# Optimization experiments

Measured on AMD Instinct MI355X. Metric: run time of the kernel, lower is better.

## Reference

```python
import jax, jax.numpy as jnp
import numpy as np

B, N, D = 64, 1024, 512
H, LD = 8, 64            # num_heads, linear_hidden_dim (H*LD == D)
HIDDEN = 4 * D           # ffn_multiply = 4.0
NB = 128                 # number of timestamp buckets
EPS = 1e-6
TS_SCALE = NB / 14.0     # log1p(1e6) ~ 13.8 -> buckets span [0, NB]


def rms_norm(x, eps=EPS):
    return x * jax.lax.rsqrt(jnp.mean(x * x, axis=-1, keepdims=True) + eps)


def setup_inputs() -> dict:
    key = jax.random.key(0)
    ks = jax.random.split(key, 8)
    lengths = np.linspace(256, N, B).astype(np.int64)
    x_offsets = jnp.asarray(np.concatenate([[0], np.cumsum(lengths)]), dtype=jnp.int64)
    T = int(lengths.sum())
    x = jax.random.normal(ks[0], (T, D), dtype=jnp.float32)
    all_timestamps = jnp.sort(jax.random.randint(ks[1], (B, N), 0, 10**6, dtype=jnp.int64), axis=1)
    invalid_attn_mask = jnp.tril(jnp.ones((N, N), jnp.float32))  # causal
    uv = jax.random.normal(ks[2], (D, 3 * H * LD), dtype=jnp.float32) * 0.02
    pos_w = jax.random.normal(ks[3], (2 * N - 1,), dtype=jnp.float32) * 0.02
    ts_w = jax.random.normal(ks[4], (NB + 1,), dtype=jnp.float32) * 0.02
    w_ams = jax.random.normal(ks[5], (2 * H * LD, D), dtype=jnp.float32) * 0.02
    w1 = jax.random.normal(ks[6], (D, HIDDEN), dtype=jnp.float32) * 0.02
    w2 = jax.random.normal(ks[7], (HIDDEN, D), dtype=jnp.float32) * 0.02
    return {"x": x, "x_offsets": x_offsets, "all_timestamps": all_timestamps,
            "invalid_attn_mask": invalid_attn_mask, "uv": uv, "pos_w": pos_w,
            "ts_w": ts_w, "w_ams": w_ams, "w1": w1, "w2": w2}


def reference(x, x_offsets, all_timestamps, invalid_attn_mask, uv, pos_w, ts_w, w_ams, w1, w2):
    T = x.shape[0]
    # RMSNorm (no learned scale, matches F.rms_norm with no weight) + fused proj + SiLU
    proj = jax.nn.silu(rms_norm(x) @ uv)                       # [T, 3*H*LD]
    u, v = proj[:, :2 * H * LD], proj[:, 2 * H * LD:]          # [T,2HD'], [T,HD']
    # jagged -> padded dense
    tok = jnp.arange(T)
    seg = jnp.searchsorted(x_offsets, tok, side="right") - 1   # batch id per token
    pos = tok - x_offsets[seg]                                  # position within sequence
    padded_v = jnp.zeros((B, N, H * LD), v.dtype).at[seg, pos].set(v).reshape(B, N, H, LD)
    # positional relative bias (batch-independent)
    rel = jnp.arange(N)[:, None] - jnp.arange(N)[None, :]
    pos_attn = pos_w[rel + N - 1] * invalid_attn_mask           # [N,N]
    # temporal relative bias: log-bucketized |t_i - t_j|
    dt = jnp.abs(all_timestamps[:, :, None] - all_timestamps[:, None, :]).astype(jnp.float32)
    bucket = jnp.clip(jnp.floor(jnp.log1p(dt) * TS_SCALE), 0, NB).astype(jnp.int32)
    ts_attn = ts_w[bucket] * invalid_attn_mask[None]            # [B,N,N]
    # two-stream bias 'attention' (no softmax)
    out_pos = jnp.einsum("nm,bmhd->bnhd", pos_attn, padded_v)
    out_ts = jnp.einsum("bnm,bmhd->bnhd", ts_attn, padded_v)
    combined = jnp.concatenate([out_pos, out_ts], axis=-1).reshape(B, N, 2 * H * LD)
    attn_out = combined[seg, pos]                               # dense -> jagged, [T, 2*H*LD]
    # gated norm + multistage FFN with residuals
    ams = u * rms_norm(attn_out)
    h = x + ams @ w_ams
    out = h + jax.nn.silu(rms_norm(h) @ w1) @ w2
    return out
```

## Files before the change

kernel.cpp:

```cpp
#include <hip/hip_runtime.h>
#include <cmath>


using u16 = unsigned short;
using u8  = unsigned char;

typedef __bf16 bf16x8 __attribute__((ext_vector_type(8)));
typedef __bf16 bf16x2 __attribute__((ext_vector_type(2)));
typedef float  f32x4  __attribute__((ext_vector_type(4)));
typedef float  f32x2  __attribute__((ext_vector_type(2)));

#define TS_SCALE_F (float)(128.0 / 14.0)

__device__ __forceinline__ u16 f2b(float f) {
  unsigned u = __float_as_uint(f);
  unsigned r = 0x7FFFu + ((u >> 16) & 1u);
  return (u16)((u + r) >> 16);
}
__device__ __forceinline__ u16 f2b_n(float f) {
  union { __bf16 b; u16 u; } c; c.b = (__bf16)f; return c.u;
}
__device__ __forceinline__ unsigned cvt_pk2(float a, float b) {
  f32x2 v; v[0] = a; v[1] = b;
  bf16x2 r = __builtin_convertvector(v, bf16x2);
  union { bf16x2 b; unsigned u; } c; c.b = r; return c.u;
}
__device__ __forceinline__ float b2f(u16 v) {
  return __uint_as_float(((unsigned)v) << 16);
}
__device__ __forceinline__ bf16x8 as_frag(uint4 r) {
  union { uint4 u; bf16x8 v; } c; c.u = r; return c.v;
}

__device__ __forceinline__ void gload_lds16(const u16* g, u16* l) {
  __builtin_amdgcn_global_load_lds(
      (const __attribute__((address_space(1))) unsigned int*)g,
      (__attribute__((address_space(3))) unsigned int*)l, 16, 0, 0);
}

__device__ __forceinline__ size_t ts_base_u8(int b, int nt) {
  return (size_t)b * 589824 + (size_t)(nt * (nt + 1) / 2) * 16384;
}

__global__ __launch_bounds__(256) void wprep(
    const float* __restrict__ W, u16* __restrict__ Wp, int K, int N)
{
  const int p = blockIdx.x, s = blockIdx.y;
  const int t = threadIdx.x;
  size_t base = ((size_t)p * (K >> 5) + s) * 4096;
  const int e0 = t * 16;
  u16 o[16];
#pragma unroll
  for (int i = 0; i < 16; ++i) {
    int e = e0 + i;
    int kb = e >> 10, r = e & 1023, c = r >> 3, ke = r & 7;
    o[i] = f2b(W[(size_t)(s * 32 + kb * 8 + ke) * N + p * 128 + c]);
  }
  *(uint4*)(Wp + base + e0)     = *(uint4*)o;
  *(uint4*)(Wp + base + e0 + 8) = *(uint4*)(o + 8);
}

#define EPI_SILU_BF16  0
#define EPI_ADD_F32    1
#define EPI_ADDS       3
#define EPI_SILUSC_IMG 4
#define AM_BF16   0
#define AM_IMG    3
#define AM_BF16M  5

template <int EPI, int AMODE>
__global__ __launch_bounds__(256, 2) void gemm_bf16(
    const u16* __restrict__ A,
    const float* __restrict__ inv, const u16* __restrict__ U, int ustride,
    const u16* __restrict__ Wp, void* __restrict__ C,
    const float* __restrict__ ADD,
    int M, int N, int K, int ncb)
{
  __shared__ u16 lA[128 * 40];
  __shared__ u16 lB[4096];

  const int nblk = gridDim.x;
  const int q = nblk >> 3, r = nblk & 7;
  const int xcd = blockIdx.x & 7, li = blockIdx.x >> 3;
  const int work = xcd * q + (xcd < r ? xcd : r) + li;
  const int c0b = work % ncb;
  const int t0  = (work / ncb) * 128;
  const int c0  = c0b * 128;

  const int tid  = threadIdx.x;
  const int wave = tid >> 6, lane = tid & 63;
  const int wr   = (wave >> 1) * 64, wc = (wave & 1) * 64;
  const int l15  = lane & 15, l4 = lane >> 4;

  f32x4 z = {0.f, 0.f, 0.f, 0.f};
  f32x4 acc[4][4];
#pragma unroll
  for (int m = 0; m < 4; ++m)
#pragma unroll
    for (int j = 0; j < 4; ++j) acc[m][j] = z;

  const int ar = tid >> 1, ak = (tid & 1) * 16;
  const int row = t0 + ar;
  const bool arow_ok = row < M;
  const u16* ab = (AMODE == AM_BF16 || AMODE == AM_BF16M)
                      ? A + (size_t)row * K + ak : nullptr;
  const u16* um = (AMODE == AM_BF16M)
                      ? U + (size_t)row * ustride + ak : nullptr;

  const int ksteps = K >> 5;
  const u16* wsrc = Wp + (size_t)c0b * ksteps * 4096 + wave * 1024 + lane * 8;
  u16* ldsb = &lB[wave * 1024];
  const u16* asrc = (AMODE == AM_IMG)
      ? A + (size_t)(t0 >> 7) * ksteps * 4096 + wave * 1024 + lane * 8
      : nullptr;
  u16* ldsa = &lA[wave * 1024];

  for (int s = 0; s < ksteps; ++s) {
    gload_lds16(wsrc,       ldsb);
    gload_lds16(wsrc + 512, ldsb + 512);
    wsrc += 4096;
    if constexpr (AMODE == AM_IMG) {
      gload_lds16(asrc,       ldsa);
      gload_lds16(asrc + 512, ldsa + 512);
      asrc += 4096;
    } else {
      const int k0 = s * 32;
      uint4 pr[4];
      const uint4 z4 = make_uint4(0, 0, 0, 0);
      if (!arow_ok) { pr[0] = z4; pr[1] = z4; pr[2] = z4; pr[3] = z4; }
      else if constexpr (AMODE == AM_BF16) {
        pr[0] = *(const uint4*)(ab + k0);
        pr[1] = *(const uint4*)(ab + k0 + 8);
      } else {
        pr[0] = *(const uint4*)(ab + k0);
        pr[1] = *(const uint4*)(ab + k0 + 8);
        pr[2] = *(const uint4*)(um + k0);
        pr[3] = *(const uint4*)(um + k0 + 8);
      }
      u16 tmp[16];
      unsigned* t32 = (unsigned*)tmp;
      if constexpr (AMODE == AM_BF16) {
        *(uint4*)tmp       = pr[0];
        *(uint4*)(tmp + 8) = pr[1];
      } else {
        const u16* a = (const u16*)pr;
        const u16* u = (const u16*)(pr + 2);
#pragma unroll
        for (int i = 0; i < 8; ++i)
          t32[i] = cvt_pk2(b2f(a[2 * i]) * b2f(u[2 * i]),
                           b2f(a[2 * i + 1]) * b2f(u[2 * i + 1]));
      }
      *(uint4*)&lA[ar * 40 + ak]     = *(uint4*)tmp;
      *(uint4*)&lA[ar * 40 + ak + 8] = *(uint4*)(tmp + 8);
    }
    __syncthreads();

    bf16x8 afr[4], bfv[4];
#pragma unroll
    for (int m = 0; m < 4; ++m) {
      if constexpr (AMODE == AM_IMG)
        afr[m] = as_frag(*(const uint4*)&lA[(l4 << 10) + (wr + m * 16 + l15) * 8]);
      else
        afr[m] = as_frag(*(const uint4*)&lA[(wr + m * 16 + l15) * 40 + l4 * 8]);
    }
#pragma unroll
    for (int j = 0; j < 4; ++j)
      bfv[j] = as_frag(*(const uint4*)&lB[(l4 << 10) + (wc + j * 16 + l15) * 8]);
#pragma unroll
    for (int m = 0; m < 4; ++m)
#pragma unroll
      for (int j = 0; j < 4; ++j)
        acc[m][j] = __builtin_amdgcn_mfma_f32_16x16x32_bf16(afr[m], bfv[j], acc[m][j], 0, 0, 0);
    __syncthreads();
  }

#pragma unroll
  for (int m = 0; m < 4; ++m) {
#pragma unroll
    for (int rr = 0; rr < 4; ++rr) {
      int orow = t0 + wr + m * 16 + l4 * 4 + rr;
      if (orow >= M) continue;
      float einv = 0.f;
      if (EPI == EPI_ADDS || EPI == EPI_SILUSC_IMG) einv = inv[orow];
#pragma unroll
      for (int j = 0; j < 4; ++j) {
        int col = c0 + wc + j * 16 + l15;
        float y = acc[m][j][rr];
        if constexpr (EPI == EPI_SILU_BF16) {
          float s = y / (1.f + __expf(-y));
          ((u16*)C)[(size_t)orow * N + col] = f2b_n(s);
        } else if constexpr (EPI == EPI_ADD_F32) {
          size_t idx = (size_t)orow * N + col;
          ((float*)C)[idx] = y + ADD[idx];
        } else if constexpr (EPI == EPI_ADDS) {
          size_t idx = (size_t)orow * N + col;
          ((float*)C)[idx] = y * einv + ADD[idx];
        } else {
          float y2 = y * einv;
          float s = y2 / (1.f + __expf(-y2));
          size_t ioff = ((size_t)(t0 >> 7) * (N >> 5) + (col >> 5)) * 4096
                      + (size_t)((col >> 3) & 3) * 1024
                      + (size_t)(orow & 127) * 8 + (col & 7);
          ((u16*)C)[ioff] = f2b_n(s);
        }
      }
    }
  }
}

__global__ __launch_bounds__(128) void pos_scores(
    const float* __restrict__ pos_w, u16* __restrict__ pos_s)
{
  const int n = blockIdx.x;
  const int m0 = threadIdx.x * 8;
  u16 o[8];
#pragma unroll
  for (int i = 0; i < 8; ++i) {
    int m = m0 + i;
    float v = (m <= n) ? pos_w[n - m + 1023] : 0.f;
    o[i] = f2b(v);
  }
  *(uint4*)(pos_s + (size_t)n * 1024 + m0) = *(uint4*)o;
}

__global__ __launch_bounds__(256) void ts_buckets(
    const int* __restrict__ tstamp, u8* __restrict__ ts_s)
{
  const int nt = 7 - (blockIdx.x >> 6);
  const int b  = blockIdx.x & 63;
  const int W  = 128 * (nt + 1);
  const int n0 = nt * 128;
  const int tid = threadIdx.x;

  __shared__ int tsm[1024];
  for (int i = tid; i < W; i += 256) tsm[i] = tstamp[b * 1024 + i];
  __syncthreads();

  const int r = tid >> 1, h = tid & 1;
  const int n_abs = n0 + r;
  const int t_n = tstamp[b * 1024 + n_abs];
  const int half = W >> 1;
  const int c0 = h * half;
  u8* row = ts_s + ts_base_u8(b, nt) + (size_t)r * W + c0;

  for (int c = 0; c < half; c += 16) {
    u8 o[16];
#pragma unroll
    for (int i = 0; i < 16; ++i) {
      int m = c0 + c + i;
      int d = t_n - tsm[m];
      if (d < 0) d = -d;
      int bkt = (int)(log1pf((float)d) * TS_SCALE_F);
      bkt = bkt > 128 ? 128 : bkt;
      o[i] = (m <= n_abs) ? (u8)bkt : (u8)129;
    }
    *(uint4*)(row + c) = *(uint4*)o;
  }
}

__global__ __launch_bounds__(256, 1) void attn_gemm(
    const u16* __restrict__ proj,
    const int* __restrict__ xoff,
    const u16* __restrict__ pos_s,
    const u8*  __restrict__ tsU8,
    const float* __restrict__ ts_w,
    u16* __restrict__ attn_out,
    int Ttot)
{
  const int flat = blockIdx.x;
  const int nt = 7 - (flat >> 8);
  const int rem = flat & 255;
  const int b  = rem >> 2;
  const int ct = rem & 3;

  const int off = xoff[b];
  int len = xoff[b + 1] - off;
  if (len < 0) len = 0;
  if (len > 1024) len = 1024;
  if (off < 0 || off + len > Ttot) return;
  const int n0 = nt * 128;
  if (n0 >= len) return;
  const int c0 = ct * 128;
  const int W = 128 * (nt + 1);

  __shared__ u16 lP[128 * 40];
  __shared__ u16 lT[128 * 40];
  __shared__ u16 sV[4096];
  __shared__ float s_tsw[130];

  const int tid = threadIdx.x;
  if (tid < 130) s_tsw[tid] = (tid < 129) ? ts_w[tid] : 0.f;
  __syncthreads();

  const int wave = tid >> 6, lane = tid & 63;
  const int wr = (wave >> 1) * 64, wc = (wave & 1) * 64;
  const int l15 = lane & 15, l4 = lane >> 4;

  f32x4 z = {0.f, 0.f, 0.f, 0.f};
  f32x4 accP[4][4], accT[4][4];
#pragma unroll
  for (int m = 0; m < 4; ++m)
#pragma unroll
    for (int j = 0; j < 4; ++j) { accP[m][j] = z; accT[m][j] = z; }

  const int ar = tid >> 1, ak = (tid & 1) * 16;
  const u16* pRow = pos_s + (size_t)(n0 + ar) * 1024 + ak;
  const u8*  tRow = tsU8 + ts_base_u8(b, nt) + (size_t)ar * W + ak;
  const int vk = tid >> 3, vc = (tid & 7) * 16;

  const int mEnd = (n0 + 128 < len) ? (n0 + 128) : len;

  for (int m0 = 0; m0 < mEnd; m0 += 32) {
    {
      int mm = m0 + vk;
      uint4 v0 = make_uint4(0, 0, 0, 0), v1 = v0;
      if (mm < len) {
        const u16* src = proj + (size_t)(off + mm) * 1536 + 1024 + c0 + vc;
        v0 = *(const uint4*)src;
        v1 = *(const uint4*)(src + 8);
      }
      u16 tmp[16];
      *(uint4*)tmp       = v0;
      *(uint4*)(tmp + 8) = v1;
      const int kb = vk >> 3, ke = vk & 7;
#pragma unroll
      for (int i = 0; i < 16; ++i) {
        int col = vc + i;
        int o2 = (kb * 2048 + col * 16 + ke * 2) ^ (((col >> 3) & 7) << 4);
        *(u16*)((char*)sV + o2) = tmp[i];
      }
    }
    {
      uint4 p0 = *(const uint4*)(pRow + m0);
      uint4 p1 = *(const uint4*)(pRow + m0 + 8);
      uint4 tb = *(const uint4*)(tRow + m0);
      const u8* bp = (const u8*)&tb;
      unsigned tt32[8];
#pragma unroll
      for (int i = 0; i < 8; ++i)
        tt32[i] = cvt_pk2(s_tsw[bp[2 * i]], s_tsw[bp[2 * i + 1]]);
      int wb = ar * 40 + ak;
      *(uint4*)&lP[wb]     = p0;
      *(uint4*)&lP[wb + 8] = p1;
      *(uint4*)&lT[wb]     = *(uint4*)tt32;
      *(uint4*)&lT[wb + 8] = *(uint4*)(tt32 + 4);
    }
    __syncthreads();

    bf16x8 ap[4], at[4], bv[4];
#pragma unroll
    for (int m = 0; m < 4; ++m) {
      ap[m] = as_frag(*(const uint4*)&lP[(wr + m * 16 + l15) * 40 + l4 * 8]);
      at[m] = as_frag(*(const uint4*)&lT[(wr + m * 16 + l15) * 40 + l4 * 8]);
    }
#pragma unroll
    for (int j = 0; j < 4; ++j) {
      int col = wc + j * 16 + l15;
      int o2 = (l4 * 2048 + col * 16) ^ (((col >> 3) & 7) << 4);
      bv[j] = as_frag(*(const uint4*)((char*)sV + o2));
    }
#pragma unroll
    for (int m = 0; m < 4; ++m)
#pragma unroll
      for (int j = 0; j < 4; ++j) {
        accP[m][j] = __builtin_amdgcn_mfma_f32_16x16x32_bf16(ap[m], bv[j], accP[m][j], 0, 0, 0);
        accT[m][j] = __builtin_amdgcn_mfma_f32_16x16x32_bf16(at[m], bv[j], accT[m][j], 0, 0, 0);
      }
    __syncthreads();
  }

#pragma unroll
  for (int m = 0; m < 4; ++m)
#pragma unroll
    for (int r = 0; r < 4; ++r) {
      int n = n0 + wr + m * 16 + l4 * 4 + r;
      if (n >= len) continue;
      size_t t = (size_t)(off + n);
#pragma unroll
      for (int j = 0; j < 4; ++j) {
        int hd = c0 + wc + j * 16 + l15;
        int colP = ((hd >> 6) << 7) + (hd & 63);
        attn_out[t * 1024 + colP]      = f2b_n(accP[m][j][r]);
        attn_out[t * 1024 + colP + 64] = f2b_n(accT[m][j][r]);
      }
    }
}

template <int D, bool F32IN, bool WIMG, bool WBF16>
__global__ __launch_bounds__(256) void row_ss(
    const void* __restrict__ in, float* __restrict__ inv, u16* __restrict__ aux,
    int T)
{
  const int row = blockIdx.x * 4 + (threadIdx.x >> 6);
  const int lane = threadIdx.x & 63;
  if (row >= T) return;
  float ss = 0.f;
  float v8[8];
  if constexpr (F32IN) {
    const float* r = (const float*)in + (size_t)row * D;
    if constexpr (WIMG || WBF16) {
      float4 a = *(const float4*)(r + lane * 8);
      float4 b = *(const float4*)(r + lane * 8 + 4);
      v8[0] = a.x; v8[1] = a.y; v8[2] = a.z; v8[3] = a.w;
      v8[4] = b.x; v8[5] = b.y; v8[6] = b.z; v8[7] = b.w;
#pragma unroll
      for (int k = 0; k < 8; ++k) ss += v8[k] * v8[k];
    } else {
#pragma unroll
      for (int i = lane * 4; i < D; i += 256) {
        float4 v = *(const float4*)(r + i);
        ss += v.x * v.x + v.y * v.y + v.z * v.z + v.w * v.w;
      }
    }
  } else {
    const u16* r = (const u16*)in + (size_t)row * D;
#pragma unroll
    for (int i = lane * 8; i < D; i += 512) {
      uint4 v = *(const uint4*)(r + i);
      const u16* q = (const u16*)&v;
#pragma unroll
      for (int k = 0; k < 8; ++k) { float f = b2f(q[k]); ss += f * f; }
    }
  }
#pragma unroll
  for (int o = 32; o > 0; o >>= 1) ss += __shfl_down(ss, o, 64);
  ss = __shfl(ss, 0, 64);
  float rv = rsqrtf(ss / (float)D + 1e-6f);
  if (lane == 0) inv[row] = rv;
  if constexpr (WIMG) {
    unsigned w[4];
#pragma unroll
    for (int i = 0; i < 4; ++i)
      w[i] = cvt_pk2(v8[2 * i] * rv, v8[2 * i + 1] * rv);
    size_t off = (size_t)(row >> 7) * ((D >> 5) * 4096)
               + (size_t)(lane >> 2) * 4096 + (size_t)(lane & 3) * 1024
               + (size_t)(row & 127) * 8;
    *(uint4*)(aux + off) = *(uint4*)w;
  } else if constexpr (WBF16) {
    unsigned w[4];
#pragma unroll
    for (int i = 0; i < 4; ++i)
      w[i] = cvt_pk2(v8[2 * i], v8[2 * i + 1]);
    *(uint4*)(aux + (size_t)row * D + lane * 8) = *(uint4*)w;
  }
}

extern "C" void kernel_launch(void* const* d_in, const int* in_sizes, int n_in,
                              void* d_out, int out_size, void* d_ws, size_t ws_size,
                              hipStream_t stream)
{
  const float* x      = (const float*)d_in[0];
  const int*   xoff   = (const int*)d_in[1];
  const int*   tstamp = (const int*)d_in[2];
  const float* uv     = (const float*)d_in[4];
  const float* pos_w  = (const float*)d_in[5];
  const float* ts_w   = (const float*)d_in[6];
  const float* w_ams  = (const float*)d_in[7];
  const float* w1     = (const float*)d_in[8];
  const float* w2     = (const float*)d_in[9];
  const int T = in_sizes[0] / 512;
  const int nrow = (T + 127) / 128;

  char* ws = (char*)d_ws;
  size_t o = 0;
  auto take = [&](size_t bytes) { size_t r = o; o += (bytes + 255) & ~(size_t)255; return r; };

  u16* uvb    = (u16*)(ws + take((size_t)512 * 1536 * 2));
  u16* wamsb  = (u16*)(ws + take((size_t)1024 * 512 * 2));
  u16* w1b    = (u16*)(ws + take((size_t)512 * 2048 * 2));
  u16* w2b    = (u16*)(ws + take((size_t)2048 * 512 * 2));
  u16* posS   = (u16*)(ws + take((size_t)1024 * 1024 * 2));

  size_t o_ts   = take((size_t)64 * 589824 + 256);
  size_t o_attn = take((size_t)T * 1024 * 2);
  size_t o_proj = take((size_t)T * 1536 * 2);
  float* invX = (float*)(ws + take((size_t)T * 4));
  float* invA = (float*)(ws + take((size_t)T * 4));
  float* invH = (float*)(ws + take((size_t)T * 4));

  u8*  tsU8  = (u8*)(ws + o_ts);
  u16* attnS = (u16*)(ws + o_attn);
  u16* proj  = (u16*)(ws + o_proj);
  u16* midI  = (u16*)(ws + o_ts);
  u16* hB    = (u16*)(ws + o_proj + (size_t)T * 2048);
  u16*   xb  = (u16*)d_out;
  float* h   = (float*)d_out;

  if (ws_size < o) return;

  wprep<<<dim3(12, 16), 256, 0, stream>>>(uv,    uvb,   512,  1536);
  wprep<<<dim3(4, 32),  256, 0, stream>>>(w_ams, wamsb, 1024, 512);
  wprep<<<dim3(16, 16), 256, 0, stream>>>(w1,    w1b,   512,  2048);
  wprep<<<dim3(4, 64),  256, 0, stream>>>(w2,    w2b,   2048, 512);

  pos_scores<<<1024, 128, 0, stream>>>(pos_w, posS);
  ts_buckets<<<512, 256, 0, stream>>>(tstamp, tsU8);

  row_ss<512, true, true, false><<<(T + 3) / 4, 256, 0, stream>>>(x, invX, xb, T);

  gemm_bf16<EPI_SILU_BF16, AM_IMG><<<12 * nrow, 256, 0, stream>>>(
      xb, nullptr, nullptr, 0, uvb, proj, nullptr, T, 1536, 512, 12);

  attn_gemm<<<64 * 32, 256, 0, stream>>>(proj, xoff, posS, tsU8, ts_w, attnS, T);

  row_ss<1024, false, false, false><<<(T + 3) / 4, 256, 0, stream>>>(
      attnS, invA, nullptr, T);

  gemm_bf16<EPI_ADDS, AM_BF16M><<<4 * nrow, 256, 0, stream>>>(
      attnS, invA, proj, 1536, wamsb, h, x, T, 512, 1024, 4);

  row_ss<512, true, false, true><<<(T + 3) / 4, 256, 0, stream>>>(h, invH, hB, T);

  gemm_bf16<EPI_SILUSC_IMG, AM_BF16><<<16 * nrow, 256, 0, stream>>>(
      hB, invH, nullptr, 0, w1b, midI, nullptr, T, 2048, 512, 16);

  gemm_bf16<EPI_ADD_F32, AM_IMG><<<4 * nrow, 256, 0, stream>>>(
      midI, nullptr, nullptr, 0, w2b, h, h, T, 512, 2048, 4);
}
```

Before: 838.8 us.

## Double-buffer LDS in image-layout GEMM and feed FFN1 pre-normalized image input

Adds a two-stage LDS double buffer to the AM_IMG GEMM path, so the next k-step's global-to-LDS loads are issued before computing the current one, with vmcnt waits and raw barriers. The h RMSNorm now writes a pre-scaled bf16 tiled image instead of a row-major bf16 copy, letting the w1 GEMM use the async image load path and drop the per-row scale in its epilogue. This aims to hide memory latency in three GEMMs at the cost of doubled LDS, which may reduce occupancy. Normalizing before the bf16 cast also changes rounding slightly.

After: 836.7 us. Within noise of the previous version (-0.3%).

```diff
diff --git a/kernel.cpp b/kernel.cpp
--- a/kernel.cpp
+++ b/kernel.cpp
@@ -62,8 +62,8 @@
 
 #define EPI_SILU_BF16  0
 #define EPI_ADD_F32    1
+#define EPI_SILU_IMG   2
 #define EPI_ADDS       3
-#define EPI_SILUSC_IMG 4
 #define AM_BF16   0
 #define AM_IMG    3
 #define AM_BF16M  5
@@ -76,8 +76,10 @@
     const float* __restrict__ ADD,
     int M, int N, int K, int ncb)
 {
-  __shared__ u16 lA[128 * 40];
-  __shared__ u16 lB[4096];
+  constexpr int NB_ = (AMODE == AM_IMG) ? 2 : 1;
+  constexpr int ASZ = (AMODE == AM_IMG) ? 4096 : 5120;
+  __shared__ u16 lA[NB_ * ASZ];
+  __shared__ u16 lB[NB_ * 4096];
 
   const int nblk = gridDim.x;
   const int q = nblk >> 3, r = nblk & 7;
@@ -99,31 +101,59 @@
 #pragma unroll
     for (int j = 0; j < 4; ++j) acc[m][j] = z;
 
-  const int ar = tid >> 1, ak = (tid & 1) * 16;
-  const int row = t0 + ar;
-  const bool arow_ok = row < M;
-  const u16* ab = (AMODE == AM_BF16 || AMODE == AM_BF16M)
-                      ? A + (size_t)row * K + ak : nullptr;
-  const u16* um = (AMODE == AM_BF16M)
-                      ? U + (size_t)row * ustride + ak : nullptr;
-
   const int ksteps = K >> 5;
   const u16* wsrc = Wp + (size_t)c0b * ksteps * 4096 + wave * 1024 + lane * 8;
-  u16* ldsb = &lB[wave * 1024];
-  const u16* asrc = (AMODE == AM_IMG)
-      ? A + (size_t)(t0 >> 7) * ksteps * 4096 + wave * 1024 + lane * 8
-      : nullptr;
-  u16* ldsa = &lA[wave * 1024];
-
-  for (int s = 0; s < ksteps; ++s) {
-    gload_lds16(wsrc,       ldsb);
-    gload_lds16(wsrc + 512, ldsb + 512);
-    wsrc += 4096;
-    if constexpr (AMODE == AM_IMG) {
-      gload_lds16(asrc,       ldsa);
-      gload_lds16(asrc + 512, ldsa + 512);
-      asrc += 4096;
-    } else {
+
+  if constexpr (AMODE == AM_IMG) {
+    const u16* asrc = A + (size_t)(t0 >> 7) * ksteps * 4096 + wave * 1024 + lane * 8;
+    auto stage = [&](int b) {
+      u16* sb = &lB[b * 4096 + wave * 1024];
+      u16* sa = &lA[b * 4096 + wave * 1024];
+      gload_lds16(wsrc,       sb);
+      gload_lds16(wsrc + 512, sb + 512);
+      gload_lds16(asrc,       sa);
+      gload_lds16(asrc + 512, sa + 512);
+      wsrc += 4096; asrc += 4096;
+    };
+    auto compute = [&](int b) {
+      bf16x8 afr[4], bfv[4];
+#pragma unroll
+      for (int m = 0; m < 4; ++m)
+        afr[m] = as_frag(*(const uint4*)&lA[b * 4096 + (l4 << 10) + (wr + m * 16 + l15) * 8]);
+#pragma unroll
+      for (int j = 0; j < 4; ++j)
+        bfv[j] = as_frag(*(const uint4*)&lB[b * 4096 + (l4 << 10) + (wc + j * 16 + l15) * 8]);
+#pragma unroll
+      for (int m = 0; m < 4; ++m)
+#pragma unroll
+        for (int j = 0; j < 4; ++j)
+          acc[m][j] = __builtin_amdgcn_mfma_f32_16x16x32_bf16(afr[m], bfv[j], acc[m][j], 0, 0, 0);
+    };
+    stage(0);
+    int buf = 0;
+    for (int s = 0; s + 1 < ksteps; ++s) {
+      stage(buf ^ 1);
+      asm volatile("s_waitcnt vmcnt(4)" ::: "memory");
+      __builtin_amdgcn_s_barrier();
+      compute(buf);
+      __builtin_amdgcn_s_barrier();
+      buf ^= 1;
+    }
+    asm volatile("s_waitcnt vmcnt(0)" ::: "memory");
+    __builtin_amdgcn_s_barrier();
+    compute(buf);
+  } else {
+    const int ar = tid >> 1, ak = (tid & 1) * 16;
+    const int row = t0 + ar;
+    const bool arow_ok = row < M;
+    const u16* ab = A + (size_t)row * K + ak;
+    const u16* um = (AMODE == AM_BF16M) ? U + (size_t)row * ustride + ak : nullptr;
+    u16* ldsb = &lB[wave * 1024];
+
+    for (int s = 0; s < ksteps; ++s) {
+      gload_lds16(wsrc,       ldsb);
+      gload_lds16(wsrc + 512, ldsb + 512);
+      wsrc += 4096;
       const int k0 = s * 32;
       uint4 pr[4];
       const uint4 z4 = make_uint4(0, 0, 0, 0);
@@ -152,26 +182,22 @@
       }
       *(uint4*)&lA[ar * 40 + ak]     = *(uint4*)tmp;
       *(uint4*)&lA[ar * 40 + ak + 8] = *(uint4*)(tmp + 8);
-    }
-    __syncthreads();
-
-    bf16x8 afr[4], bfv[4];
-#pragma unroll
-    for (int m = 0; m < 4; ++m) {
-      if constexpr (AMODE == AM_IMG)
-        afr[m] = as_frag(*(const uint4*)&lA[(l4 << 10) + (wr + m * 16 + l15) * 8]);
-      else
+      __syncthreads();
+
+      bf16x8 afr[4], bfv[4];
+#pragma unroll
+      for (int m = 0; m < 4; ++m)
         afr[m] = as_frag(*(const uint4*)&lA[(wr + m * 16 + l15) * 40 + l4 * 8]);
-    }
-#pragma unroll
-    for (int j = 0; j < 4; ++j)
-      bfv[j] = as_frag(*(const uint4*)&lB[(l4 << 10) + (wc + j * 16 + l15) * 8]);
-#pragma unroll
-    for (int m = 0; m < 4; ++m)
 #pragma unroll
       for (int j = 0; j < 4; ++j)
-        acc[m][j] = __builtin_amdgcn_mfma_f32_16x16x32_bf16(afr[m], bfv[j], acc[m][j], 0, 0, 0);
-    __syncthreads();
+        bfv[j] = as_frag(*(const uint4*)&lB[(l4 << 10) + (wc + j * 16 + l15) * 8]);
+#pragma unroll
+      for (int m = 0; m < 4; ++m)
+#pragma unroll
+        for (int j = 0; j < 4; ++j)
+          acc[m][j] = __builtin_amdgcn_mfma_f32_16x16x32_bf16(afr[m], bfv[j], acc[m][j], 0, 0, 0);
+      __syncthreads();
+    }
   }
 
 #pragma unroll
@@ -181,7 +207,7 @@
       int orow = t0 + wr + m * 16 + l4 * 4 + rr;
       if (orow >= M) continue;
       float einv = 0.f;
-      if (EPI == EPI_ADDS || EPI == EPI_SILUSC_IMG) einv = inv[orow];
+      if (EPI == EPI_ADDS) einv = inv[orow];
 #pragma unroll
       for (int j = 0; j < 4; ++j) {
         int col = c0 + wc + j * 16 + l15;
@@ -196,8 +222,7 @@
           size_t idx = (size_t)orow * N + col;
           ((float*)C)[idx] = y * einv + ADD[idx];
         } else {
-          float y2 = y * einv;
-          float s = y2 / (1.f + __expf(-y2));
+          float s = y / (1.f + __expf(-y));
           size_t ioff = ((size_t)(t0 >> 7) * (N >> 5) + (col >> 5)) * 4096
                       + (size_t)((col >> 3) & 3) * 1024
                       + (size_t)(orow & 127) * 8 + (col & 7);
@@ -386,7 +411,7 @@
     }
 }
 
-template <int D, bool F32IN, bool WIMG, bool WBF16>
+template <int D, bool F32IN, bool WIMG>
 __global__ __launch_bounds__(256) void row_ss(
     const void* __restrict__ in, float* __restrict__ inv, u16* __restrict__ aux,
     int T)
@@ -398,7 +423,7 @@
   float v8[8];
   if constexpr (F32IN) {
     const float* r = (const float*)in + (size_t)row * D;
-    if constexpr (WIMG || WBF16) {
+    if constexpr (WIMG) {
       float4 a = *(const float4*)(r + lane * 8);
       float4 b = *(const float4*)(r + lane * 8 + 4);
       v8[0] = a.x; v8[1] = a.y; v8[2] = a.z; v8[3] = a.w;
@@ -436,12 +461,6 @@
                + (size_t)(lane >> 2) * 4096 + (size_t)(lane & 3) * 1024
                + (size_t)(row & 127) * 8;
     *(uint4*)(aux + off) = *(uint4*)w;
-  } else if constexpr (WBF16) {
-    unsigned w[4];
-#pragma unroll
-    for (int i = 0; i < 4; ++i)
-      w[i] = cvt_pk2(v8[2 * i], v8[2 * i + 1]);
-    *(uint4*)(aux + (size_t)row * D + lane * 8) = *(uint4*)w;
   }
 }
 
@@ -473,7 +492,7 @@
 
   size_t o_ts   = take((size_t)64 * 589824 + 256);
   size_t o_attn = take((size_t)T * 1024 * 2);
-  size_t o_proj = take((size_t)T * 1536 * 2);
+  size_t o_proj = take((size_t)T * 1536 * 2 + 131072);
   float* invX = (float*)(ws + take((size_t)T * 4));
   float* invA = (float*)(ws + take((size_t)T * 4));
   float* invH = (float*)(ws + take((size_t)T * 4));
@@ -482,7 +501,7 @@
   u16* attnS = (u16*)(ws + o_attn);
   u16* proj  = (u16*)(ws + o_proj);
   u16* midI  = (u16*)(ws + o_ts);
-  u16* hB    = (u16*)(ws + o_proj + (size_t)T * 2048);
+  u16* hImg  = (u16*)(ws + o_proj + (size_t)T * 2048);
   u16*   xb  = (u16*)d_out;
   float* h   = (float*)d_out;
 
@@ -496,23 +515,23 @@
   pos_scores<<<1024, 128, 0, stream>>>(pos_w, posS);
   ts_buckets<<<512, 256, 0, stream>>>(tstamp, tsU8);
 
-  row_ss<512, true, true, false><<<(T + 3) / 4, 256, 0, stream>>>(x, invX, xb, T);
+  row_ss<512, true, true><<<(T + 3) / 4, 256, 0, stream>>>(x, invX, xb, T);
 
   gemm_bf16<EPI_SILU_BF16, AM_IMG><<<12 * nrow, 256, 0, stream>>>(
       xb, nullptr, nullptr, 0, uvb, proj, nullptr, T, 1536, 512, 12);
 
   attn_gemm<<<64 * 32, 256, 0, stream>>>(proj, xoff, posS, tsU8, ts_w, attnS, T);
 
-  row_ss<1024, false, false, false><<<(T + 3) / 4, 256, 0, stream>>>(
+  row_ss<1024, false, false><<<(T + 3) / 4, 256, 0, stream>>>(
       attnS, invA, nullptr, T);
 
   gemm_bf16<EPI_ADDS, AM_BF16M><<<4 * nrow, 256, 0, stream>>>(
       attnS, invA, proj, 1536, wamsb, h, x, T, 512, 1024, 4);
 
-  row_ss<512, true, false, true><<<(T + 3) / 4, 256, 0, stream>>>(h, invH, hB, T);
-
-  gemm_bf16<EPI_SILUSC_IMG, AM_BF16><<<16 * nrow, 256, 0, stream>>>(
-      hB, invH, nullptr, 0, w1b, midI, nullptr, T, 2048, 512, 16);
+  row_ss<512, true, true><<<(T + 3) / 4, 256, 0, stream>>>(h, invH, hImg, T);
+
+  gemm_bf16<EPI_SILU_IMG, AM_IMG><<<16 * nrow, 256, 0, stream>>>(
+      hImg, nullptr, nullptr, 0, w1b, midI, nullptr, T, 2048, 512, 16);
 
   gemm_bf16<EPI_ADD_F32, AM_IMG><<<4 * nrow, 256, 0, stream>>>(
       midI, nullptr, nullptr, 0, w2b, h, h, T, 512, 2048, 4);
```
